# Optimization experiments

Hardware: AMD Instinct MI355X
Metric: run time of the kernel (lower is better)

## Reference

```python
import jax, jax.numpy as jnp
import numpy as np

NODE_W, EDGE_W, HEADS = 512, 32, 8
DOT = NODE_W // HEADS
CLIP_MIN, CLIP_MAX = -5.0, 5.0
B, N = 4, 1024


def setup_inputs() -> dict:
    key = jax.random.key(0)
    ks = jax.random.split(key, 12)
    s = 0.02
    return {
        "nodes": jax.random.normal(ks[0], (B, N, NODE_W), dtype=jnp.float32),
        "edges": jax.random.normal(ks[1], (B, N, N, EDGE_W), dtype=jnp.float32),
        "Wq": jax.random.normal(ks[2], (NODE_W, NODE_W), dtype=jnp.float32) * s,
        "bq": jnp.zeros((NODE_W,), dtype=jnp.float32),
        "Wk": jax.random.normal(ks[3], (NODE_W, NODE_W), dtype=jnp.float32) * s,
        "bk": jnp.zeros((NODE_W,), dtype=jnp.float32),
        "Wv": jax.random.normal(ks[4], (NODE_W, NODE_W), dtype=jnp.float32) * s,
        "bv": jnp.zeros((NODE_W,), dtype=jnp.float32),
        "Wg": jax.random.normal(ks[5], (EDGE_W, HEADS), dtype=jnp.float32) * s,
        "bg": jnp.zeros((HEADS,), dtype=jnp.float32),
        "We": jax.random.normal(ks[6], (EDGE_W, HEADS), dtype=jnp.float32) * s,
        "be": jnp.zeros((HEADS,), dtype=jnp.float32),
    }


def reference(nodes, edges, Wq, bq, Wk, bk, Wv, bv, Wg, bg, We, be):
    b, n, _ = nodes.shape
    # projections, reshaped to [B, N, dot_dim, heads] as in the torch .view
    q = (nodes @ Wq + bq).reshape(b, n, DOT, HEADS)
    k = (nodes @ Wk + bk).reshape(b, n, DOT, HEADS)
    v = (nodes @ Wv + bv).reshape(b, n, DOT, HEADS)
    # raw scores [B, L, M, heads], scaled and clipped
    H = jnp.einsum('bldh,bmdh->blmh', q, k) / (DOT ** 0.5)
    H = jnp.clip(H, CLIP_MIN, CLIP_MAX)
    # edge bias and gate, each [B, N, N, heads]
    e = edges @ We + be
    g = edges @ Wg + bg
    H = H + e
    # softmax over key axis (dim=2), sigmoid gate multiply
    A = jax.nn.sigmoid(g) * jax.nn.softmax(H, axis=2)
    # dropout is identity in eval/deterministic mode
    attn = jnp.einsum('blmh,bmdh->bldh', A, v).reshape(b, n, NODE_W)
    return attn, H
```

## Files before the change

kernel.cpp:

```cpp
#include <hip/hip_runtime.h>
#include <hip/hip_bf16.h>
#include <stdint.h>

typedef float  f32x4  __attribute__((ext_vector_type(4)));
typedef float  f32x2  __attribute__((ext_vector_type(2)));
typedef short  bf16x8 __attribute__((ext_vector_type(8)));
typedef short  bf16x4 __attribute__((ext_vector_type(4)));

#define MFMA16(A,B,C) __builtin_amdgcn_mfma_f32_16x16x32_bf16(A,B,C,0,0,0)

__device__ __forceinline__ short f2bf(float x){
    union { float f; uint32_t u; } v; v.f = x;
    uint32_t r = v.u + 0x7fffu + ((v.u >> 16) & 1u);
    return (short)(r >> 16);
}
__device__ __forceinline__ float bf2f(short x){
    union { uint32_t u; float f; } v; v.u = ((uint32_t)(uint16_t)x) << 16;
    return v.f;
}
__device__ __forceinline__ bf16x8 pack8(f32x4 a, f32x4 b){
    bf16x8 r;
    r[0]=f2bf(a[0]); r[1]=f2bf(a[1]); r[2]=f2bf(a[2]); r[3]=f2bf(a[3]);
    r[4]=f2bf(b[0]); r[5]=f2bf(b[1]); r[6]=f2bf(b[2]); r[7]=f2bf(b[3]);
    return r;
}

__global__ void k_prep_wt(const float* __restrict__ Wq, const float* __restrict__ Wk,
                          const float* __restrict__ Wv, short* __restrict__ WT){
    int blk = blockIdx.x;
    int w  = blk >> 6;
    int t  = blk & 63;
    int k0 = (t >> 3) << 6;
    int o0 = (t & 7) << 6;
    const float* W = (w == 0) ? Wq : ((w == 1) ? Wk : Wv);
    __shared__ float tile[64][65];
    int tx = threadIdx.x & 63, ty = threadIdx.x >> 6;
    #pragma unroll
    for (int i = 0; i < 64; i += 4)
        tile[ty + i][tx] = W[(size_t)(k0 + ty + i) * 512 + o0 + tx];
    __syncthreads();
    short* out = WT + (size_t)w * 512 * 512;
    #pragma unroll
    for (int i = 0; i < 64; i += 4)
        out[(size_t)(o0 + ty + i) * 512 + k0 + tx] = f2bf(tile[tx][ty + i]);
}

__global__ void k_prep_wcat(const float* __restrict__ We, const float* __restrict__ Wg,
                            const float* __restrict__ be, const float* __restrict__ bg,
                            short* __restrict__ WcatT, float* __restrict__ bcat){
    int t = threadIdx.x;
    int ch = t >> 5, c = t & 31;
    float v = (ch < 8) ? We[c * 8 + ch] : Wg[c * 8 + (ch - 8)];
    WcatT[ch * 32 + c] = f2bf(v);
    if (t < 16) bcat[t] = (t < 8) ? be[t] : bg[t - 8];
}

__global__ void k_prep_nodes(const float* __restrict__ nodes, short* __restrict__ nb){
    size_t i = ((size_t)blockIdx.x * 256 + threadIdx.x) * 8;
    f32x4 a = *(const f32x4*)(nodes + i);
    f32x4 b = *(const f32x4*)(nodes + i + 4);
    *(bf16x8*)(nb + i) = pack8(a, b);
}

__global__ void k_qkv(const short* __restrict__ nodesbf, const short* __restrict__ WT,
                      const float* __restrict__ bq, const float* __restrict__ bk,
                      const float* __restrict__ bv,
                      short* __restrict__ qb, short* __restrict__ kb, short* __restrict__ vTb){
    int bx = blockIdx.x;
    int lt = bx & 255;
    int ob = bx >> 8;
    int wave = threadIdx.x >> 6, lane = threadIdx.x & 63;
    int lr = lane & 15, lg = lane >> 4;
    int row0 = lt << 4;
    int og = ob * 256 + wave * 64;
    int w  = og >> 9;
    int oo = og & 511;
    int dhalf = ob & 1;

    const short* Wp = WT + (size_t)w * 512 * 512;
    f32x4 acc[4] = {};
    const short* arow = nodesbf + (size_t)(row0 + lr) * 512 + lg * 8;
    #pragma unroll
    for (int kk = 0; kk < 16; ++kk){
        bf16x8 af = *(const bf16x8*)(arow + kk * 32);
        #pragma unroll
        for (int s = 0; s < 4; ++s){
            const short* bp = Wp + (size_t)(oo + s * 16 + lr) * 512 + kk * 32 + lg * 8;
            bf16x8 bfv = *(const bf16x8*)bp;
            acc[s] = MFMA16(af, bfv, acc[s]);
        }
    }
    const float* bias = (w == 0) ? bq : ((w == 1) ? bk : bv);
    int b  = row0 >> 10;
    int lbase = row0 & 1023;

    __shared__ short St[4096];
    #pragma unroll
    for (int s = 0; s < 4; ++s){
        int o = oo + s * 16 + lr;
        float bsv = bias[o];
        int h = o & 7, dd = (o >> 3) & 31;
        #pragma unroll
        for (int r = 0; r < 4; ++r){
            short sv = f2bf(acc[s][r] + bsv);
            int l = lg * 4 + r;
            if (w < 2) St[(l << 8) + (h << 5) + dd] = sv;
            else       St[(h << 9) + (dd << 4) + l] = sv;
        }
    }
    __syncthreads();
    int t = threadIdx.x;
    bf16x8 v0 = *(const bf16x8*)&St[t * 16];
    bf16x8 v1 = *(const bf16x8*)&St[t * 16 + 8];
    if (w < 2){
        short* dst = (w == 0) ? qb : kb;
        int l = t >> 4, h = (t >> 1) & 7, dd0 = (t & 1) << 4;
        size_t a = ((size_t)(b * 8 + h) * 1024 + lbase + l) * 64 + dhalf * 32 + dd0;
        *(bf16x8*)(dst + a)     = v0;
        *(bf16x8*)(dst + a + 8) = v1;
    } else {
        int h = t >> 5, dd = t & 31;
        size_t a = ((size_t)(b * 8 + h) * 64 + dhalf * 32 + dd) * 1024 + lbase;
        *(bf16x8*)(vTb + a)     = v0;
        *(bf16x8*)(vTb + a + 8) = v1;
    }
}

__global__ __launch_bounds__(256, 4) void k_hsg(
        const float* __restrict__ edges, const short* __restrict__ qb,
        const short* __restrict__ kb, const short* __restrict__ WcatT,
        const float* __restrict__ bcat,
        float* __restrict__ Hout, short* __restrict__ Pb,
        float* __restrict__ psum){
    int bx = blockIdx.x;
    int j  = bx & 7;  int b = j >> 1;
    int rest = bx >> 3;
    int mt = rest & 15;
    int lt = (rest >> 4) | ((j & 1) << 5);
    int w = threadIdx.x >> 6, lane = threadIdx.x & 63;
    int lr = lane & 15, lg = lane >> 4;
    int l0 = lt << 4;
    int mg = (mt << 6) + (w << 4);
    const size_t bl0 = (size_t)(b * 1024 + l0);

    __shared__ short eg[4][4][16][24];
    __shared__ float Hst[4][512];
    __shared__ short Ps[4][2048];
    __shared__ float den[4][128];

    f32x4 S[8] = {};
    #pragma unroll
    for (int h = 0; h < 8; ++h){
        #pragma unroll
        for (int half = 0; half < 2; ++half){
            bf16x8 qf = *(const bf16x8*)(qb + ((size_t)(b * 8 + h) * 1024 + l0 + lr) * 64 + half * 32 + lg * 8);
            bf16x8 kf = *(const bf16x8*)(kb + ((size_t)(b * 8 + h) * 1024 + mg + lr) * 64 + half * 32 + lg * 8);
            S[h] = MFMA16(qf, kf, S[h]);
        }
    }

    bf16x8 wf = *(const bf16x8*)(WcatT + lr * 32 + lg * 8);
    f32x4  bc = *(const f32x4*)(bcat + lg * 4);
    f32x4 zero = {0.f, 0.f, 0.f, 0.f};

    #pragma unroll
    for (int r = 0; r < 4; ++r){
        #pragma unroll
        for (int s = 0; s < 4; ++s){
            int l = 4 * s + r;
            const float* ep = edges + ((bl0 + l) * 1024 + mg + lr) * 32 + lg * 8;
            f32x4 e0 = *(const f32x4*)ep;
            f32x4 e1 = *(const f32x4*)(ep + 4);
            f32x4 d = MFMA16(wf, pack8(e0, e1), zero);
            bf16x4 dv;
            #pragma unroll
            for (int rr = 0; rr < 4; ++rr) dv[rr] = f2bf(d[rr] + bc[rr]);
            *(bf16x4*)&eg[w][s][lr][lg * 4] = dv;
        }
        int l = 4 * lg + r;
        bf16x8 e8 = *(const bf16x8*)&eg[w][lg][lr][0];
        bf16x8 g8 = *(const bf16x8*)&eg[w][lg][lr][8];
        float Hv[8], ex[8];
        #pragma unroll
        for (int h = 0; h < 8; ++h){
            float s = S[h][r] * 0.125f;
            s = fminf(fmaxf(s, -5.f), 5.f);
            Hv[h] = s + bf2f(e8[h]);
            ex[h] = __expf(Hv[h]);
            float sg = __builtin_amdgcn_rcpf(1.f + __expf(-bf2f(g8[h])));
            Ps[w][(h << 8) + (l << 4) + lr] = f2bf(ex[h] * sg);
        }
        #pragma unroll
        for (int h = 0; h < 8; ++h){
            float t = ex[h];
            t += __shfl_xor(t, 1);
            t += __shfl_xor(t, 2);
            t += __shfl_xor(t, 4);
            t += __shfl_xor(t, 8);
            if (lr == 0) den[w][(h << 4) + l] = t;
        }
        f32x4 h0 = {Hv[0], Hv[1], Hv[2], Hv[3]};
        f32x4 h1 = {Hv[4], Hv[5], Hv[6], Hv[7]};
        *(f32x4*)&Hst[w][lg * 128 + lr * 8]     = h0;
        *(f32x4*)&Hst[w][lg * 128 + lr * 8 + 4] = h1;
        f32x4 o0 = *(const f32x4*)&Hst[w][lane * 4];
        f32x4 o1 = *(const f32x4*)&Hst[w][256 + lane * 4];
        int off = (lane * 4) & 127;
        *(f32x4*)(Hout + (bl0 + 4 * (lane >> 5) + r)       * 8192 + mg * 8 + off) = o0;
        *(f32x4*)(Hout + (bl0 + 4 * ((lane >> 5) + 2) + r) * 8192 + mg * 8 + off) = o1;
    }

    #pragma unroll
    for (int jj = 0; jj < 4; ++jj){
        int f = jj * 512 + lane * 8;
        int h = f >> 8;
        bf16x8 pv = *(const bf16x8*)&Ps[w][f];
        size_t a = (((size_t)(b * 8 + h) * 64 + lt) * 64 + (mt * 4 + w)) * 256 + (f & 255);
        *(bf16x8*)(Pb + a) = pv;
    }
    {
        f32x2 dv = *(const f32x2*)&den[w][lane * 2];
        size_t a = (((size_t)(b * 64 + lt) * 16 + mt) * 4 + w) * 128 + lane * 2;
        *(f32x2*)(psum + a) = dv;
    }
}

__global__ void k_pv(const short* __restrict__ Pb, const float* __restrict__ psum,
                     const short* __restrict__ vTb, float* __restrict__ attn){
    int bx = blockIdx.x;
    int j  = bx & 7;  int b = j >> 1;
    int lt = ((j & 1) << 5) | (bx >> 3);
    int h    = threadIdx.x >> 6;
    int lane = threadIdx.x & 63;
    int lr = lane & 15, lg = lane >> 4;
    int l0 = lt << 4;

    const short* Pbase = Pb  + (((size_t)(b * 8 + h) * 64 + lt) * 64) * 256;
    const short* vbase = vTb + (size_t)(b * 8 + h) * 65536;

    f32x4 O[4] = {};
    for (int ks = 0; ks < 32; ++ks){
        bf16x8 pf = *(const bf16x8*)(Pbase + (ks * 2 + (lg >> 1)) * 256 + lr * 16 + (lg & 1) * 8);
        #pragma unroll
        for (int dt = 0; dt < 4; ++dt){
            bf16x8 vf = *(const bf16x8*)(vbase + (size_t)(dt * 16 + lr) * 1024 + ks * 32 + lg * 8);
            O[dt] = MFMA16(vf, pf, O[dt]);
        }
    }

    const float* pp = psum + ((size_t)(b * 64 + lt) * 16) * 512;
    float ds = 0.f;
    #pragma unroll
    for (int c = 0; c < 16; ++c)
        ds += pp[(c * 4 + lg) * 128 + h * 16 + lr];
    ds += __shfl_xor(ds, 16);
    ds += __shfl_xor(ds, 32);
    float inv = __builtin_amdgcn_rcpf(ds);

    __shared__ float Os[16][516];
    #pragma unroll
    for (int dt = 0; dt < 4; ++dt){
        #pragma unroll
        for (int r = 0; r < 4; ++r)
            Os[lr][(dt * 16 + lg * 4 + r) * 8 + h] = O[dt][r] * inv;
    }
    __syncthreads();
    int row = threadIdx.x >> 5;
    int cb  = (threadIdx.x & 31) * 16;
    float* dst = attn + ((size_t)(b * 1024 + l0 + row)) * 512 + cb;
    #pragma unroll
    for (int jj = 0; jj < 16; jj += 4)
        *(f32x4*)(dst + jj) = *(const f32x4*)&Os[row][cb + jj];
}

#define OFF_WT    ((size_t)0x0000000)
#define OFF_WCAT  ((size_t)0x0180000)
#define OFF_BCAT  ((size_t)0x0180400)
#define OFF_NB    ((size_t)0x0200000)
#define OFF_Q     ((size_t)0x0600000)
#define OFF_K     ((size_t)0x0A00000)
#define OFF_VT    ((size_t)0x0E00000)
#define OFF_P     ((size_t)0x1200000)
#define OFF_PS    ((size_t)0x5200000)

extern "C" void kernel_launch(void* const* d_in, const int* in_sizes, int n_in,
                              void* d_out, int out_size, void* d_ws, size_t ws_size,
                              hipStream_t stream) {
    const float* nodes = (const float*)d_in[0];
    const float* edges = (const float*)d_in[1];
    const float* Wq = (const float*)d_in[2];
    const float* bq = (const float*)d_in[3];
    const float* Wk = (const float*)d_in[4];
    const float* bk = (const float*)d_in[5];
    const float* Wv = (const float*)d_in[6];
    const float* bv = (const float*)d_in[7];
    const float* Wg = (const float*)d_in[8];
    const float* bg = (const float*)d_in[9];
    const float* We = (const float*)d_in[10];
    const float* be = (const float*)d_in[11];

    float* out_attn = (float*)d_out;
    float* out_H    = out_attn + (size_t)4 * 1024 * 512;

    char* ws = (char*)d_ws;
    short* WT    = (short*)(ws + OFF_WT);
    short* WcatT = (short*)(ws + OFF_WCAT);
    float* bcat  = (float*)(ws + OFF_BCAT);
    short* nb    = (short*)(ws + OFF_NB);
    short* qb    = (short*)(ws + OFF_Q);
    short* kb    = (short*)(ws + OFF_K);
    short* vTb   = (short*)(ws + OFF_VT);
    short* Pb    = (short*)(ws + OFF_P);
    float* psum  = (float*)(ws + OFF_PS);

    k_prep_wt   <<<192, 256, 0, stream>>>(Wq, Wk, Wv, WT);
    k_prep_wcat <<<1, 512, 0, stream>>>(We, Wg, be, bg, WcatT, bcat);
    k_prep_nodes<<<1024, 256, 0, stream>>>(nodes, nb);
    k_qkv       <<<1536, 256, 0, stream>>>(nb, WT, bq, bk, bv, qb, kb, vTb);
    k_hsg       <<<4096, 256, 0, stream>>>(edges, qb, kb, WcatT, bcat, out_H, Pb, psum);
    k_pv        <<<256, 512, 0, stream>>>(Pb, psum, vTb, out_attn);
}
```

Baseline: 293.8 us.

## Restructure edge-score kernel with register prefetch, transposed MFMA and direct stores

The fused score/softmax-numerator kernel now double-buffers edge loads in registers so the next four rows are in flight while the current ones are projected. The QK MFMA operands are swapped, so each lane holds a row layout that lets H and P be written straight to global memory. This removes the shared-memory staging for H, P and the denominators, and turns the denominator reduction into two cross-lane shuffles. Edge projections go to an XOR-swizzled shared buffer, and bf16 conversion uses the packed two-value intrinsic. Occupancy drops from 4 to 3 blocks per SIMD to make room for the extra registers.

```diff
diff --git a/kernel.cpp b/kernel.cpp
--- a/kernel.cpp
+++ b/kernel.cpp
@@ -18,11 +18,15 @@
     union { uint32_t u; float f; } v; v.u = ((uint32_t)(uint16_t)x) << 16;
     return v.f;
 }
+__device__ __forceinline__ uint32_t cvt2(float lo, float hi){
+    __hip_bfloat162 t = __float22bfloat162_rn(float2{lo, hi});
+    union { __hip_bfloat162 b; uint32_t u; } c; c.b = t; return c.u;
+}
 __device__ __forceinline__ bf16x8 pack8(f32x4 a, f32x4 b){
-    bf16x8 r;
-    r[0]=f2bf(a[0]); r[1]=f2bf(a[1]); r[2]=f2bf(a[2]); r[3]=f2bf(a[3]);
-    r[4]=f2bf(b[0]); r[5]=f2bf(b[1]); r[6]=f2bf(b[2]); r[7]=f2bf(b[3]);
-    return r;
+    union { uint32_t u[4]; bf16x8 s; } c;
+    c.u[0] = cvt2(a[0], a[1]); c.u[1] = cvt2(a[2], a[3]);
+    c.u[2] = cvt2(b[0], b[1]); c.u[3] = cvt2(b[2], b[3]);
+    return c.s;
 }
 
 __global__ void k_prep_wt(const float* __restrict__ Wq, const float* __restrict__ Wk,
@@ -126,7 +130,7 @@
     }
 }
 
-__global__ __launch_bounds__(256, 4) void k_hsg(
+__global__ __launch_bounds__(256, 3) void k_hsg(
         const float* __restrict__ edges, const short* __restrict__ qb,
         const short* __restrict__ kb, const short* __restrict__ WcatT,
         const float* __restrict__ bcat,
@@ -143,85 +147,93 @@
     int mg = (mt << 6) + (w << 4);
     const size_t bl0 = (size_t)(b * 1024 + l0);
 
-    __shared__ short eg[4][4][16][24];
-    __shared__ float Hst[4][512];
-    __shared__ short Ps[4][2048];
-    __shared__ float den[4][128];
+    __shared__ short eg[4][4096];
+    char* egw = (char*)&eg[w][0];
+    const int swz = (lr & 7) << 4;
+
+    f32x4 ebA[4][2], ebB[4][2];
+    #pragma unroll
+    for (int i = 0; i < 4; ++i){
+        const float* ep = edges + ((bl0 + i) * 1024 + mg + lr) * 32 + lg * 8;
+        ebA[i][0] = *(const f32x4*)ep;
+        ebA[i][1] = *(const f32x4*)(ep + 4);
+    }
 
     f32x4 S[8] = {};
     #pragma unroll
     for (int h = 0; h < 8; ++h){
         #pragma unroll
         for (int half = 0; half < 2; ++half){
+            bf16x8 kf = *(const bf16x8*)(kb + ((size_t)(b * 8 + h) * 1024 + mg + lr) * 64 + half * 32 + lg * 8);
             bf16x8 qf = *(const bf16x8*)(qb + ((size_t)(b * 8 + h) * 1024 + l0 + lr) * 64 + half * 32 + lg * 8);
-            bf16x8 kf = *(const bf16x8*)(kb + ((size_t)(b * 8 + h) * 1024 + mg + lr) * 64 + half * 32 + lg * 8);
-            S[h] = MFMA16(qf, kf, S[h]);
+            S[h] = MFMA16(kf, qf, S[h]);
         }
     }
 
     bf16x8 wf = *(const bf16x8*)(WcatT + lr * 32 + lg * 8);
     f32x4  bc = *(const f32x4*)(bcat + lg * 4);
     f32x4 zero = {0.f, 0.f, 0.f, 0.f};
-
-    #pragma unroll
-    for (int r = 0; r < 4; ++r){
-        #pragma unroll
-        for (int s = 0; s < 4; ++s){
-            int l = 4 * s + r;
-            const float* ep = edges + ((bl0 + l) * 1024 + mg + lr) * 32 + lg * 8;
-            f32x4 e0 = *(const f32x4*)ep;
-            f32x4 e1 = *(const f32x4*)(ep + 4);
+    #pragma unroll
+    for (int c = 0; c < 4; ++c){
+        if (c < 3){
+            #pragma unroll
+            for (int i = 0; i < 4; ++i){
+                const float* ep = edges + ((bl0 + (c + 1) * 4 + i) * 1024 + mg + lr) * 32 + lg * 8;
+                if (c & 1){ ebA[i][0] = *(const f32x4*)ep; ebA[i][1] = *(const f32x4*)(ep + 4); }
+                else      { ebB[i][0] = *(const f32x4*)ep; ebB[i][1] = *(const f32x4*)(ep + 4); }
+            }
+        }
+        #pragma unroll
+        for (int i = 0; i < 4; ++i){
+            int l = c * 4 + i;
+            f32x4 e0 = (c & 1) ? ebB[i][0] : ebA[i][0];
+            f32x4 e1 = (c & 1) ? ebB[i][1] : ebA[i][1];
             f32x4 d = MFMA16(wf, pack8(e0, e1), zero);
-            bf16x4 dv;
-            #pragma unroll
-            for (int rr = 0; rr < 4; ++rr) dv[rr] = f2bf(d[rr] + bc[rr]);
-            *(bf16x4*)&eg[w][s][lr][lg * 4] = dv;
-        }
-        int l = 4 * lg + r;
-        bf16x8 e8 = *(const bf16x8*)&eg[w][lg][lr][0];
-        bf16x8 g8 = *(const bf16x8*)&eg[w][lg][lr][8];
-        float Hv[8], ex[8];
+            union { uint32_t u[2]; bf16x4 v; } dv;
+            dv.u[0] = cvt2(d[0] + bc[0], d[1] + bc[1]);
+            dv.u[1] = cvt2(d[2] + bc[2], d[3] + bc[3]);
+            int bw = (l * 512 + lr * 32 + lg * 8) ^ ((l & 7) << 4);
+            *(bf16x4*)(egw + bw) = dv.v;
+        }
+    }
+
+    float exu[4][8], pgv[4][8];
+    #pragma unroll
+    for (int rr = 0; rr < 4; ++rr){
+        int base = lr * 512 + (4 * lg + rr) * 32;
+        bf16x8 e8 = *(const bf16x8*)(egw + ((base)      ^ swz));
+        bf16x8 g8 = *(const bf16x8*)(egw + ((base + 16) ^ swz));
+        float Hv[8];
         #pragma unroll
         for (int h = 0; h < 8; ++h){
-            float s = S[h][r] * 0.125f;
+            float s = S[h][rr] * 0.125f;
             s = fminf(fmaxf(s, -5.f), 5.f);
-            Hv[h] = s + bf2f(e8[h]);
-            ex[h] = __expf(Hv[h]);
+            float hv = s + bf2f(e8[h]);
+            Hv[h] = hv;
+            float ex = __expf(hv);
+            exu[rr][h] = ex;
             float sg = __builtin_amdgcn_rcpf(1.f + __expf(-bf2f(g8[h])));
-            Ps[w][(h << 8) + (l << 4) + lr] = f2bf(ex[h] * sg);
-        }
-        #pragma unroll
-        for (int h = 0; h < 8; ++h){
-            float t = ex[h];
-            t += __shfl_xor(t, 1);
-            t += __shfl_xor(t, 2);
-            t += __shfl_xor(t, 4);
-            t += __shfl_xor(t, 8);
-            if (lr == 0) den[w][(h << 4) + l] = t;
-        }
+            pgv[rr][h] = ex * sg;
+        }
+        float* hp = Hout + (bl0 + lr) * 8192 + (size_t)(mg + 4 * lg + rr) * 8;
         f32x4 h0 = {Hv[0], Hv[1], Hv[2], Hv[3]};
         f32x4 h1 = {Hv[4], Hv[5], Hv[6], Hv[7]};
-        *(f32x4*)&Hst[w][lg * 128 + lr * 8]     = h0;
-        *(f32x4*)&Hst[w][lg * 128 + lr * 8 + 4] = h1;
-        f32x4 o0 = *(const f32x4*)&Hst[w][lane * 4];
-        f32x4 o1 = *(const f32x4*)&Hst[w][256 + lane * 4];
-        int off = (lane * 4) & 127;
-        *(f32x4*)(Hout + (bl0 + 4 * (lane >> 5) + r)       * 8192 + mg * 8 + off) = o0;
-        *(f32x4*)(Hout + (bl0 + 4 * ((lane >> 5) + 2) + r) * 8192 + mg * 8 + off) = o1;
-    }
-
-    #pragma unroll
-    for (int jj = 0; jj < 4; ++jj){
-        int f = jj * 512 + lane * 8;
-        int h = f >> 8;
-        bf16x8 pv = *(const bf16x8*)&Ps[w][f];
-        size_t a = (((size_t)(b * 8 + h) * 64 + lt) * 64 + (mt * 4 + w)) * 256 + (f & 255);
-        *(bf16x8*)(Pb + a) = pv;
-    }
-    {
-        f32x2 dv = *(const f32x2*)&den[w][lane * 2];
-        size_t a = (((size_t)(b * 64 + lt) * 16 + mt) * 4 + w) * 128 + lane * 2;
-        *(f32x2*)(psum + a) = dv;
+        *(f32x4*)hp       = h0;
+        *(f32x4*)(hp + 4) = h1;
+    }
+
+    size_t ptile = ((size_t)(b * 8) * 64 + lt) * 64 + (mt * 4 + w);
+    size_t psbase = (((size_t)(b * 64 + lt) * 16 + mt) * 4 + w) * 128;
+    #pragma unroll
+    for (int h = 0; h < 8; ++h){
+        union { uint32_t u[2]; bf16x4 v; } pv;
+        pv.u[0] = cvt2(pgv[0][h], pgv[1][h]);
+        pv.u[1] = cvt2(pgv[2][h], pgv[3][h]);
+        *(bf16x4*)(Pb + (ptile + (size_t)h * 4096) * 256 + lr * 16 + lg * 4) = pv.v;
+        float t = exu[0][h] + exu[1][h] + exu[2][h] + exu[3][h];
+        t += __shfl_xor(t, 16);
+        t += __shfl_xor(t, 32);
+        if (lg == 0) psum[psbase + h * 16 + lr] = t;
     }
 }
 
```

After: 296.1 us. Within noise of the previous version (+0.8%).
